# Optimization experiments

Hardware: AMD Instinct MI355X
Metric: run time of the kernel (lower is better)

Reference implementation:

```python
import jax, jax.numpy as jnp
import numpy as np

BETA = 0.9
THR = 1.0
B, T, F, H = 64, 256, 1024, 512

# snntorch heaviside spike with ATan surrogate gradient (alpha=2.0, snntorch default)
@jax.custom_vjp
def spike_fn(u):
    return (u > 0).astype(u.dtype)

def _spike_fwd(u):
    return spike_fn(u), u

def _spike_bwd(u, g):
    alpha = 2.0
    grad = (alpha / 2.0) / (1.0 + (jnp.pi / 2.0 * alpha * u) ** 2)
    return (g * grad,)

spike_fn.defvjp(_spike_fwd, _spike_bwd)


def setup_inputs() -> dict:
    key = jax.random.key(0)
    ks = jax.random.split(key, 12)
    s = 0.05
    return {
        "f_f": jax.random.normal(ks[0], (B, T, F), dtype=jnp.float32),
        "seq_len": jnp.full((B,), T, dtype=jnp.int64),
        "Wf": jax.random.normal(ks[1], (H, F), dtype=jnp.float32) * s,
        "bf": jnp.zeros((H,), jnp.float32),
        "W1": jax.random.normal(ks[2], (H, H), dtype=jnp.float32) * s,
        "b1": jnp.zeros((H,), jnp.float32),
        "W2": jax.random.normal(ks[3], (H, H), dtype=jnp.float32) * s,
        "b2": jnp.zeros((H,), jnp.float32),
        "Mw1": jax.random.normal(ks[4], (512, H), dtype=jnp.float32) * s,
        "Mb1": jnp.zeros((512,), jnp.float32),
        "Mw2": jax.random.normal(ks[5], (32, 512), dtype=jnp.float32) * s,
        "Mb2": jnp.zeros((32,), jnp.float32),
        "Mw3": jax.random.normal(ks[6], (1, 32), dtype=jnp.float32) * s,
        "Mb3": jnp.zeros((1,), jnp.float32),
    }


def _forward(f_f, Wf, bf, W1, b1, W2, b2, Mw1, Mb1, Mw2, Mb2, Mw3, Mb3):
    h = f_f @ Wf.T + bf            # [B,T,H] fc_f
    x1 = h @ W1.T + b1             # layer-1 linear drive precomputed (state-independent)

    def step(carry, x1_t):
        m1, m2 = carry
        # snntorch Leaky (subtract reset): reset from previous mem's spike
        r1 = spike_fn(m1 - THR)
        m1 = BETA * m1 + x1_t - r1 * THR
        s1 = spike_fn(m1 - THR)
        x2 = s1 @ W2.T + b2        # layer-2 linear on spikes (dropout=identity, eval)
        r2 = spike_fn(m2 - THR)
        m2 = BETA * m2 + x2 - r2 * THR
        s2 = spike_fn(m2 - THR)
        return (m1, m2), s2

    init = (jnp.zeros((B, H), h.dtype), jnp.zeros((B, H), h.dtype))
    _, spk = jax.lax.scan(step, init, jnp.swapaxes(x1, 0, 1))  # [T,B,H]
    spk = jnp.swapaxes(spk, 0, 1)                              # [B,T,H]

    z = jax.nn.relu(spk @ Mw1.T + Mb1)
    z = z @ Mw2.T + Mb2
    logits = jax.nn.sigmoid((z @ Mw3.T + Mb3).squeeze(-1))     # [B,T]

    # filter: top-(seq_len//16 + 1) mean per clip; seq_len == T for all clips
    k = T // 16 + 1
    topv, _ = jax.lax.top_k(logits, k)
    return jnp.mean(topv, axis=-1)                             # [B]


def reference(f_f, seq_len, Wf, bf, W1, b1, W2, b2, Mw1, Mb1, Mw2, Mb2, Mw3, Mb3):
    return _forward(f_f, Wf, bf, W1, b1, W2, b2, Mw1, Mb1, Mw2, Mb2, Mw3, Mb3)
```

## Files before the change

### kernel.cpp

```cpp
#include <hip/hip_runtime.h>
#include <math.h>

#define BETA 0.9f
#define THR 1.0f

constexpr int B_ = 64, T_ = 256, F_ = 1024, H_ = 512;
constexpr int M_ = B_ * T_;

typedef float f32x4 __attribute__((ext_vector_type(4)));
typedef short short8 __attribute__((ext_vector_type(8)));
typedef _Float16 half8 __attribute__((ext_vector_type(8)));
typedef unsigned short us4 __attribute__((ext_vector_type(4)));
typedef unsigned short us8 __attribute__((ext_vector_type(8)));
typedef unsigned short ushort_t;

static __device__ __forceinline__ unsigned short f2bf(float x) {
    unsigned b = __builtin_bit_cast(unsigned, x);
    unsigned r = (b + 0x7FFFu + ((b >> 16) & 1u)) >> 16;
    return (unsigned short)r;
}
static __device__ __forceinline__ float bf2f(unsigned short u) {
    unsigned v = ((unsigned)u) << 16;
    return __builtin_bit_cast(float, v);
}
static __device__ __forceinline__ unsigned short f2h(float x) {
    _Float16 h = (_Float16)x;
    return __builtin_bit_cast(unsigned short, h);
}
static __device__ __forceinline__ float h2f(unsigned short u) {
    return (float)__builtin_bit_cast(_Float16, u);
}
static __device__ __forceinline__ int swz(int r) {
    return ((r >> 2) & 3) ^ (r & 3);
}

#define GLDS(srcp, dstp)                                                      \
    __builtin_amdgcn_global_load_lds(                                         \
        (const __attribute__((address_space(1))) unsigned int*)(srcp),        \
        (__attribute__((address_space(3))) unsigned int*)(dstp), 16, 0, 0)

template <int AF32>
__global__ __launch_bounds__(512, 4) void gemm_scan(
    const void* __restrict__ Asrc, const ushort_t* __restrict__ Bp,
    const float* __restrict__ bias, ushort_t* __restrict__ Sout, int K) {
    constexpr int BUF = 20480;
    __shared__ ushort_t lds[2 * BUF];

    const int tid = threadIdx.x;
    const int w = tid >> 6, l = tid & 63;
    const int flat = blockIdx.y * gridDim.x + blockIdx.x;
    const int clip = ((flat >> 6) << 3) | (flat & 7);
    const int strip = (flat >> 3) & 7;
    const int n0 = strip * 64;
    const int m0 = clip * 256;

    f32x4 acc[2][4];
#pragma unroll
    for (int mi = 0; mi < 2; ++mi)
#pragma unroll
        for (int ni = 0; ni < 4; ++ni) acc[mi][ni] = (f32x4){0.f, 0.f, 0.f, 0.f};

    const int c0 = l >> 4;
    const int schunk = (l & 7) ^ ((l >> 3) & 7);

    f32x4 areg[4][2];

    auto stageB = [&](int buf, int k0) {
        const int r = w * 8 + (l >> 3);
        GLDS(Bp + (size_t)(n0 + r) * K + k0 + schunk * 8,
             &lds[buf + 16384 + w * 512]);
    };
    auto stageA16 = [&](int buf, int k0) {
#pragma unroll
        for (int j = 0; j < 4; ++j) {
            const int seg = w * 4 + j;
            const int r = seg * 8 + (l >> 3);
            GLDS((const ushort_t*)Asrc + (size_t)(m0 + r) * K + k0 + schunk * 8,
                 &lds[buf + seg * 512]);
        }
    };
    auto loadA32 = [&](int k0) {
#pragma unroll
        for (int j = 0; j < 4; ++j) {
            const int r = j * 64 + (tid >> 3);
            const float* src =
                (const float*)Asrc + (size_t)(m0 + r) * K + k0 + (tid & 7) * 8;
            areg[j][0] = *(const f32x4*)src;
            areg[j][1] = *(const f32x4*)(src + 4);
        }
    };
    auto writeA32 = [&](int buf) {
#pragma unroll
        for (int j = 0; j < 4; ++j) {
            const int r = j * 64 + (tid >> 3);
            us8 hv;
#pragma unroll
            for (int e = 0; e < 4; ++e) {
                hv[e] = f2h(areg[j][0][e]);
                hv[e + 4] = f2h(areg[j][1][e]);
            }
            const int pos = (tid & 7) ^ (r & 7);
            *(us8*)&lds[buf + r * 64 + pos * 8] = hv;
        }
    };

    const int nt = K / 64;
    if constexpr (AF32) {
        loadA32(0);
        writeA32(0);
    } else {
        stageA16(0, 0);
    }
    stageB(0, 0);

    for (int t = 0; t < nt; ++t) {
        const int cur = (t & 1) * BUF;
        const int nxt = BUF - cur;
        __syncthreads();
        const bool more = (t + 1 < nt);
        if (more) {
            if constexpr (AF32) {
                loadA32((t + 1) * 64);
                stageB(nxt, (t + 1) * 64);
            } else {
                stageA16(nxt, (t + 1) * 64);
                stageB(nxt, (t + 1) * 64);
            }
        }

#pragma unroll
        for (int kh = 0; kh < 2; ++kh) {
            half8 aa[2], bb[4];
            const int q = kh * 4 + c0;
#pragma unroll
            for (int mi = 0; mi < 2; ++mi) {
                const int r = w * 32 + mi * 16 + (l & 15);
                const int off = cur + r * 64 + ((q ^ (l & 7)) * 8);
                aa[mi] = __builtin_bit_cast(half8, *(const short8*)&lds[off]);
            }
#pragma unroll
            for (int ni = 0; ni < 4; ++ni) {
                const int r = ni * 16 + (l & 15);
                const int off = cur + 16384 + r * 64 + ((q ^ (l & 7)) * 8);
                bb[ni] = __builtin_bit_cast(half8, *(const short8*)&lds[off]);
            }
#pragma unroll
            for (int mi = 0; mi < 2; ++mi)
#pragma unroll
                for (int ni = 0; ni < 4; ++ni)
                    acc[mi][ni] = __builtin_amdgcn_mfma_f32_16x16x32_f16(
                        aa[mi], bb[ni], acc[mi][ni], 0, 0, 0);
        }

        if constexpr (AF32) {
            if (more) writeA32(nxt);
        }
    }

    float bv[4];
#pragma unroll
    for (int ni = 0; ni < 4; ++ni) bv[ni] = bias[n0 + ni * 16 + (l & 15)];
#pragma unroll
    for (int mi = 0; mi < 2; ++mi) {
        const int t0 = w * 32 + mi * 16 + ((l >> 4) << 2);
#pragma unroll
        for (int ni = 0; ni < 4; ++ni) {
            const int h = ni * 16 + (l & 15);
#pragma unroll
            for (int r = 0; r < 4; ++r)
                lds[(t0 + r) * 66 + h] = f2h(acc[mi][ni][r] + bv[ni]);
        }
    }
    __syncthreads();

    if (tid < 64) {
        const int h = tid;
        ushort_t* sp = Sout + (size_t)m0 * 512 + n0 + h;
        float m = 0.f;
#pragma unroll 4
        for (int t = 0; t < T_; ++t) {
            const float xv = h2f(lds[t * 66 + h]);
            const float r = (m - THR > 0.f) ? THR : 0.f;
            m = BETA * m + xv - r;
            sp[(size_t)t * 512] = (m - THR > 0.f) ? (ushort_t)0x3C00 : (ushort_t)0;
        }
    }
}

__global__ __launch_bounds__(256) void gemm_mil(
    const ushort_t* __restrict__ Ap, const ushort_t* __restrict__ Bp,
    const float* __restrict__ bias, const float* __restrict__ Uv,
    float* __restrict__ part, int N, int K) {
    constexpr int BUF = 16384;
    __shared__ ushort_t lds[2 * BUF];

    const int tid = threadIdx.x;
    const int w = tid >> 6, l = tid & 63;
    const int flat = blockIdx.y * gridDim.x + blockIdx.x;
    const int mt = ((flat >> 5) << 3) | (flat & 7);
    const int st = (flat >> 3) & 3;
    const int n0 = st * 128;
    const int m0 = mt * 128;
    const int wr = w >> 1, wc = w & 1;

    f32x4 acc[4][4];
#pragma unroll
    for (int mi = 0; mi < 4; ++mi)
#pragma unroll
        for (int ni = 0; ni < 4; ++ni) acc[mi][ni] = (f32x4){0.f, 0.f, 0.f, 0.f};

    const int c0 = l >> 4;
    const int schunk = (l & 7) ^ ((l >> 3) & 7);

    auto stage = [&](int buf, int k0) {
#pragma unroll
        for (int j = 0; j < 8; ++j) {
            const int g = w * 8 + j;
            const int seg = g & 15;
            const int r = seg * 8 + (l >> 3);
            const ushort_t* pl = (g < 16) ? Ap : Bp;
            const int rb = (g < 16) ? m0 : n0;
            GLDS(pl + (size_t)(rb + r) * K + k0 + schunk * 8,
                 &lds[buf + g * 512]);
        }
    };

    const int nt = K / 64;
    stage(0, 0);
    for (int t = 0; t < nt; ++t) {
        const int cur = (t & 1) * BUF;
        const int nxt = BUF - cur;
        __syncthreads();
        if (t + 1 < nt) stage(nxt, (t + 1) * 64);

#pragma unroll
        for (int kh = 0; kh < 2; ++kh) {
            half8 aa[4], bb[4];
            const int q = kh * 4 + c0;
#pragma unroll
            for (int mi = 0; mi < 4; ++mi) {
                const int r = wr * 64 + mi * 16 + (l & 15);
                const int off = cur + r * 64 + ((q ^ (l & 7)) * 8);
                aa[mi] = __builtin_bit_cast(half8, *(const short8*)&lds[off]);
            }
#pragma unroll
            for (int ni = 0; ni < 4; ++ni) {
                const int r = wc * 64 + ni * 16 + (l & 15);
                const int off = cur + 8192 + r * 64 + ((q ^ (l & 7)) * 8);
                bb[ni] = __builtin_bit_cast(half8, *(const short8*)&lds[off]);
            }
#pragma unroll
            for (int mi = 0; mi < 4; ++mi)
#pragma unroll
                for (int ni = 0; ni < 4; ++ni)
                    acc[mi][ni] = __builtin_amdgcn_mfma_f32_16x16x32_f16(
                        aa[mi], bb[ni], acc[mi][ni], 0, 0, 0);
        }
    }

    float bv[4], uc[4];
#pragma unroll
    for (int ni = 0; ni < 4; ++ni) {
        const int col = n0 + wc * 64 + ni * 16 + (l & 15);
        bv[ni] = bias[col];
        uc[ni] = Uv[col];
    }
    const int strip = (n0 >> 6) + wc;
#pragma unroll
    for (int mi = 0; mi < 4; ++mi) {
        float p[4];
#pragma unroll
        for (int r = 0; r < 4; ++r) {
            float s = 0.f;
#pragma unroll
            for (int ni = 0; ni < 4; ++ni)
                s += fmaxf(acc[mi][ni][r] + bv[ni], 0.f) * uc[ni];
            p[r] = s;
        }
#pragma unroll
        for (int off = 1; off <= 8; off <<= 1)
#pragma unroll
            for (int r = 0; r < 4; ++r) p[r] += __shfl_xor(p[r], off);
        if ((l & 15) == 0) {
            const int row0 = m0 + wr * 64 + mi * 16 + ((l >> 4) << 2);
#pragma unroll
            for (int r = 0; r < 4; ++r)
                part[(size_t)strip * M_ + row0 + r] = p[r];
        }
    }
}

__global__ __launch_bounds__(256) void gemm_bf16_wc(
    const ushort_t* __restrict__ Ah, const ushort_t* __restrict__ Al,
    const ushort_t* __restrict__ Bh, const ushort_t* __restrict__ Bl,
    ushort_t* __restrict__ Cout, int N, int K) {
    __shared__ ushort_t lds[4 * 4096];

    const int tid = threadIdx.x;
    const int w = tid >> 6, l = tid & 63;
    const int nwg = gridDim.x * gridDim.y;
    const int flat = blockIdx.y * gridDim.x + blockIdx.x;
    const int wg = (flat & 7) * (nwg >> 3) + (flat >> 3);
    const int n0 = (wg % gridDim.x) * 128;
    const int m0 = (wg / gridDim.x) * 128;
    const int wr = w >> 1, wc = w & 1;

    f32x4 acc[4][4];
#pragma unroll
    for (int mi = 0; mi < 4; ++mi)
#pragma unroll
        for (int ni = 0; ni < 4; ++ni) acc[mi][ni] = (f32x4){0.f, 0.f, 0.f, 0.f};

    const int c0 = l >> 4;
    for (int k0 = 0; k0 < K; k0 += 32) {
        __syncthreads();
#pragma unroll
        for (int j = 0; j < 8; ++j) {
            const int g = w * 8 + j;
            const int p = g >> 3, seg = g & 7;
            const int r = seg * 16 + (l >> 2);
            const int ch = (l & 3) ^ swz(r);
            const ushort_t* pl = (p == 0) ? Ah : (p == 1) ? Al : (p == 2) ? Bh : Bl;
            const int rb = (p < 2) ? m0 : n0;
            GLDS(pl + (size_t)(rb + r) * K + k0 + ch * 8,
                 &lds[p * 4096 + seg * 512]);
        }
        __syncthreads();

        short8 ah[4], al[4], bh[4], bl[4];
#pragma unroll
        for (int mi = 0; mi < 4; ++mi) {
            const int r = wr * 64 + mi * 16 + (l & 15);
            const int off = r * 32 + ((c0 ^ swz(r)) * 8);
            ah[mi] = *(const short8*)&lds[off];
            al[mi] = *(const short8*)&lds[4096 + off];
        }
#pragma unroll
        for (int ni = 0; ni < 4; ++ni) {
            const int r = wc * 64 + ni * 16 + (l & 15);
            const int off = r * 32 + ((c0 ^ swz(r)) * 8);
            bh[ni] = *(const short8*)&lds[8192 + off];
            bl[ni] = *(const short8*)&lds[12288 + off];
        }
#pragma unroll
        for (int mi = 0; mi < 4; ++mi)
#pragma unroll
            for (int ni = 0; ni < 4; ++ni) {
                acc[mi][ni] = __builtin_amdgcn_mfma_f32_16x16x32_bf16(
                    ah[mi], bh[ni], acc[mi][ni], 0, 0, 0);
                acc[mi][ni] = __builtin_amdgcn_mfma_f32_16x16x32_bf16(
                    ah[mi], bl[ni], acc[mi][ni], 0, 0, 0);
                acc[mi][ni] = __builtin_amdgcn_mfma_f32_16x16x32_bf16(
                    al[mi], bh[ni], acc[mi][ni], 0, 0, 0);
            }
    }

#pragma unroll
    for (int ni = 0; ni < 4; ++ni) {
        const int col = n0 + wc * 64 + ni * 16 + (l & 15);
#pragma unroll
        for (int mi = 0; mi < 4; ++mi) {
            const int row0 = m0 + wr * 64 + mi * 16 + ((l >> 4) << 2);
#pragma unroll
            for (int r = 0; r < 4; ++r)
                Cout[(size_t)(row0 + r) * N + col] = f2h(acc[mi][ni][r]);
        }
    }
}

__global__ __launch_bounds__(256) void prep_small(
    const float* __restrict__ W1, const float* __restrict__ W2,
    const float* __restrict__ Mw1, const float* __restrict__ bfv,
    const float* __restrict__ b1, const float* __restrict__ Mw2,
    const float* __restrict__ Mb2, const float* __restrict__ Mw3,
    const float* __restrict__ Mb3, const float* __restrict__ Wf,
    ushort_t* __restrict__ w1h, ushort_t* __restrict__ w1l,
    ushort_t* __restrict__ w2f, ushort_t* __restrict__ m1f,
    float* __restrict__ bc, float* __restrict__ uc,
    ushort_t* __restrict__ wfTh, ushort_t* __restrict__ wfTl) {
    __shared__ float tile[32][33];
    const int blk = blockIdx.x;
    const int tid = threadIdx.x;
    if (blk < 256) {
        const int i = blk * 256 + tid;
        f32x4 v = ((const f32x4*)W1)[i];
        us4 h, ll;
#pragma unroll
        for (int e = 0; e < 4; ++e) {
            const unsigned short hb = f2bf(v[e]);
            h[e] = hb;
            ll[e] = f2bf(v[e] - bf2f(hb));
        }
        ((us4*)w1h)[i] = h;
        ((us4*)w1l)[i] = ll;
    } else if (blk < 512) {
        const int i = (blk - 256) * 256 + tid;
        f32x4 v = ((const f32x4*)W2)[i];
        us4 h;
#pragma unroll
        for (int e = 0; e < 4; ++e) h[e] = f2h(v[e]);
        ((us4*)w2f)[i] = h;
    } else if (blk < 768) {
        const int i = (blk - 512) * 256 + tid;
        f32x4 v = ((const f32x4*)Mw1)[i];
        us4 h;
#pragma unroll
        for (int e = 0; e < 4; ++e) h[e] = f2h(v[e]);
        ((us4*)m1f)[i] = h;
    } else if (blk < 896) {
        const int w = tid >> 6, l = tid & 63;
        const int j = (blk - 768) * 4 + w;
        const float* row = W1 + (size_t)j * 512;
        float a = 0.f;
#pragma unroll
        for (int i = 0; i < 8; ++i) a += row[l + i * 64] * bfv[l + i * 64];
#pragma unroll
        for (int off = 32; off >= 1; off >>= 1) a += __shfl_xor(a, off);
        if (l == 0) bc[j] = a + b1[j];
    } else if (blk < 898) {
        const int j = (blk - 896) * 256 + tid;
        float a = 0.f;
        for (int i = 0; i < 32; ++i) a += Mw3[i] * Mw2[(size_t)i * 512 + j];
        uc[j] = a;
        if (j == 0) {
            float c = Mb3[0];
            for (int i = 0; i < 32; ++i) c += Mw3[i] * Mb2[i];
            uc[512] = c;
        }
    } else {
        const int idx = blk - 898;
        const int k0 = (idx & 31) * 32;
        const int i0 = (idx >> 5) * 32;
        const int tx = tid & 31;
        const int ty = tid >> 5;
#pragma unroll
        for (int e = 0; e < 4; ++e) {
            const int i = ty + e * 8;
            tile[i][tx] = Wf[(size_t)(i0 + i) * 1024 + k0 + tx];
        }
        __syncthreads();
#pragma unroll
        for (int e = 0; e < 4; ++e) {
            const int kk = ty + e * 8;
            const float v = tile[tx][kk];
            const unsigned short h = f2bf(v);
            wfTh[(size_t)(k0 + kk) * 512 + i0 + tx] = h;
            wfTl[(size_t)(k0 + kk) * 512 + i0 + tx] = f2bf(v - bf2f(h));
        }
    }
}

__global__ __launch_bounds__(64) void tail_topk(const float* __restrict__ part,
                                                const float* __restrict__ uc,
                                                float* __restrict__ out) {
    const int b = blockIdx.x;
    const int lane = threadIdx.x;
    const float c = uc[512];
    float v[4];
#pragma unroll
    for (int i = 0; i < 4; ++i) {
        const int row = b * T_ + lane + i * 64;
        float a = 0.f;
#pragma unroll
        for (int s = 0; s < 8; ++s) a += part[(size_t)s * M_ + row];
        v[i] = a + c;
    }
    float sum = 0.f;
    for (int iter = 0; iter < 17; ++iter) {
        float mv = v[0];
        int mslot = 0;
#pragma unroll
        for (int i = 1; i < 4; ++i)
            if (v[i] > mv) { mv = v[i]; mslot = i; }
        float bv = mv;
        int bl = lane, bs = mslot;
#pragma unroll
        for (int off = 32; off >= 1; off >>= 1) {
            const float ov = __shfl_xor(bv, off);
            const int ol = __shfl_xor(bl, off);
            const int os = __shfl_xor(bs, off);
            if (ov > bv || (ov == bv && ol < bl)) { bv = ov; bl = ol; bs = os; }
        }
        sum += 1.f / (1.f + expf(-bv));
        if (lane == bl) v[bs] = -1e30f;
    }
    if (lane == 0) out[b] = sum * (1.f / 17.f);
}

extern "C" void kernel_launch(void* const* d_in, const int* in_sizes, int n_in,
                              void* d_out, int out_size, void* d_ws, size_t ws_size,
                              hipStream_t stream) {
    const float* f_f = (const float*)d_in[0];
    const float* Wf  = (const float*)d_in[2];
    const float* bf  = (const float*)d_in[3];
    const float* W1  = (const float*)d_in[4];
    const float* b1  = (const float*)d_in[5];
    const float* W2  = (const float*)d_in[6];
    const float* b2  = (const float*)d_in[7];
    const float* Mw1 = (const float*)d_in[8];
    const float* Mb1 = (const float*)d_in[9];
    const float* Mw2 = (const float*)d_in[10];
    const float* Mb2 = (const float*)d_in[11];
    const float* Mw3 = (const float*)d_in[12];
    const float* Mb3 = (const float*)d_in[13];
    float* out = (float*)d_out;

    char* ws = (char*)d_ws;
    const size_t NE = (size_t)M_ * H_;
    ushort_t* sbuf1 = (ushort_t*)ws;
    ushort_t* sbuf2 = sbuf1 + NE;
    ushort_t* w1h = sbuf2 + NE;
    ushort_t* w1l = w1h + 262144;
    ushort_t* w2f = w1l + 262144;
    ushort_t* m1f = w2f + 262144;
    ushort_t* wfTh = m1f + 262144;
    ushort_t* wfTl = wfTh + 524288;
    ushort_t* wcf = wfTl + 524288;
    float* bc = (float*)(wcf + 524288);
    float* uc = bc + 512;
    float* part = uc + 513 + 63;

    const dim3 blk(256);

    prep_small<<<dim3(1410), blk, 0, stream>>>(W1, W2, Mw1, bf, b1, Mw2, Mb2,
                                               Mw3, Mb3, Wf, w1h, w1l, w2f,
                                               m1f, bc, uc, wfTh, wfTl);

    gemm_bf16_wc<<<dim3(8, 4), blk, 0, stream>>>(w1h, w1l, wfTh, wfTl, wcf,
                                                 1024, 512);
    gemm_scan<1><<<dim3(8, 64), dim3(512), 0, stream>>>(f_f, wcf, bc, sbuf1,
                                                        1024);
    gemm_scan<0><<<dim3(8, 64), dim3(512), 0, stream>>>(sbuf1, w2f, b2, sbuf2,
                                                        512);
    gemm_mil<<<dim3(4, 128), blk, 0, stream>>>(sbuf2, m1f, Mb1, uc, part,
                                               512, 512);
    tail_topk<<<dim3(B_), dim3(64), 0, stream>>>(part, uc, out);
}
```

Baseline: 112.3 us.

## Double-buffer split-bf16 GEMM with 64-wide K tiles and raise MFMA wave priority

Rewrites the bf16 hi/lo GEMM main loop to double-buffer LDS with K tiles of 64, so global-to-LDS loads for the next tile overlap the MFMAs on the current one, and drops one barrier per iteration. It changes the LDS swizzle, raises launch bounds to one block, and removes the workgroup remapping used for L2 locality. It also wraps the MFMA blocks in all GEMMs with s_setprio to favour math-issuing waves. The cost is more LDS per block (128KB), which limits occupancy, and possibly worse cache locality without the remap.

```diff
diff --git a/kernel.cpp b/kernel.cpp
--- a/kernel.cpp
+++ b/kernel.cpp
@@ -144,12 +144,14 @@
                 const int off = cur + 16384 + r * 64 + ((q ^ (l & 7)) * 8);
                 bb[ni] = __builtin_bit_cast(half8, *(const short8*)&lds[off]);
             }
+            __builtin_amdgcn_s_setprio(1);
 #pragma unroll
             for (int mi = 0; mi < 2; ++mi)
 #pragma unroll
                 for (int ni = 0; ni < 4; ++ni)
                     acc[mi][ni] = __builtin_amdgcn_mfma_f32_16x16x32_f16(
                         aa[mi], bb[ni], acc[mi][ni], 0, 0, 0);
+            __builtin_amdgcn_s_setprio(0);
         }
 
         if constexpr (AF32) {
@@ -249,12 +251,14 @@
                 const int off = cur + 8192 + r * 64 + ((q ^ (l & 7)) * 8);
                 bb[ni] = __builtin_bit_cast(half8, *(const short8*)&lds[off]);
             }
+            __builtin_amdgcn_s_setprio(1);
 #pragma unroll
             for (int mi = 0; mi < 4; ++mi)
 #pragma unroll
                 for (int ni = 0; ni < 4; ++ni)
                     acc[mi][ni] = __builtin_amdgcn_mfma_f32_16x16x32_f16(
                         aa[mi], bb[ni], acc[mi][ni], 0, 0, 0);
+            __builtin_amdgcn_s_setprio(0);
         }
     }
 
@@ -290,19 +294,18 @@
     }
 }
 
-__global__ __launch_bounds__(256) void gemm_bf16_wc(
+__global__ __launch_bounds__(256, 1) void gemm_bf16_wc(
     const ushort_t* __restrict__ Ah, const ushort_t* __restrict__ Al,
     const ushort_t* __restrict__ Bh, const ushort_t* __restrict__ Bl,
     ushort_t* __restrict__ Cout, int N, int K) {
-    __shared__ ushort_t lds[4 * 4096];
+    constexpr int BUF = 32768;
+    __shared__ ushort_t lds[2 * BUF];
 
     const int tid = threadIdx.x;
     const int w = tid >> 6, l = tid & 63;
-    const int nwg = gridDim.x * gridDim.y;
     const int flat = blockIdx.y * gridDim.x + blockIdx.x;
-    const int wg = (flat & 7) * (nwg >> 3) + (flat >> 3);
-    const int n0 = (wg % gridDim.x) * 128;
-    const int m0 = (wg / gridDim.x) * 128;
+    const int n0 = (flat % gridDim.x) * 128;
+    const int m0 = (flat / gridDim.x) * 128;
     const int wr = w >> 1, wc = w & 1;
 
     f32x4 acc[4][4];
@@ -312,47 +315,61 @@
         for (int ni = 0; ni < 4; ++ni) acc[mi][ni] = (f32x4){0.f, 0.f, 0.f, 0.f};
 
     const int c0 = l >> 4;
-    for (int k0 = 0; k0 < K; k0 += 32) {
-        __syncthreads();
-#pragma unroll
-        for (int j = 0; j < 8; ++j) {
-            const int g = w * 8 + j;
-            const int p = g >> 3, seg = g & 7;
-            const int r = seg * 16 + (l >> 2);
-            const int ch = (l & 3) ^ swz(r);
+    const int schunk = (l & 7) ^ ((l >> 3) & 7);
+
+    auto stage = [&](int buf, int k0) {
+#pragma unroll
+        for (int j = 0; j < 16; ++j) {
+            const int g = w * 16 + j;
+            const int p = g >> 4, seg = g & 15;
+            const int r = seg * 8 + (l >> 3);
             const ushort_t* pl = (p == 0) ? Ah : (p == 1) ? Al : (p == 2) ? Bh : Bl;
             const int rb = (p < 2) ? m0 : n0;
-            GLDS(pl + (size_t)(rb + r) * K + k0 + ch * 8,
-                 &lds[p * 4096 + seg * 512]);
-        }
+            GLDS(pl + (size_t)(rb + r) * K + k0 + schunk * 8,
+                 &lds[buf + g * 512]);
+        }
+    };
+
+    const int nt = K / 64;
+    stage(0, 0);
+    for (int t = 0; t < nt; ++t) {
+        const int cur = (t & 1) * BUF;
+        const int nxt = BUF - cur;
         __syncthreads();
-
-        short8 ah[4], al[4], bh[4], bl[4];
-#pragma unroll
-        for (int mi = 0; mi < 4; ++mi) {
-            const int r = wr * 64 + mi * 16 + (l & 15);
-            const int off = r * 32 + ((c0 ^ swz(r)) * 8);
-            ah[mi] = *(const short8*)&lds[off];
-            al[mi] = *(const short8*)&lds[4096 + off];
-        }
-#pragma unroll
-        for (int ni = 0; ni < 4; ++ni) {
-            const int r = wc * 64 + ni * 16 + (l & 15);
-            const int off = r * 32 + ((c0 ^ swz(r)) * 8);
-            bh[ni] = *(const short8*)&lds[8192 + off];
-            bl[ni] = *(const short8*)&lds[12288 + off];
-        }
-#pragma unroll
-        for (int mi = 0; mi < 4; ++mi)
+        if (t + 1 < nt) stage(nxt, (t + 1) * 64);
+
+#pragma unroll
+        for (int kh = 0; kh < 2; ++kh) {
+            short8 ah[4], al[4], bh[4], bl[4];
+            const int q = kh * 4 + c0;
+#pragma unroll
+            for (int mi = 0; mi < 4; ++mi) {
+                const int r = wr * 64 + mi * 16 + (l & 15);
+                const int off = r * 64 + ((q ^ (l & 7)) * 8);
+                ah[mi] = *(const short8*)&lds[cur + off];
+                al[mi] = *(const short8*)&lds[cur + 8192 + off];
+            }
 #pragma unroll
             for (int ni = 0; ni < 4; ++ni) {
-                acc[mi][ni] = __builtin_amdgcn_mfma_f32_16x16x32_bf16(
-                    ah[mi], bh[ni], acc[mi][ni], 0, 0, 0);
-                acc[mi][ni] = __builtin_amdgcn_mfma_f32_16x16x32_bf16(
-                    ah[mi], bl[ni], acc[mi][ni], 0, 0, 0);
-                acc[mi][ni] = __builtin_amdgcn_mfma_f32_16x16x32_bf16(
-                    al[mi], bh[ni], acc[mi][ni], 0, 0, 0);
-            }
+                const int r = wc * 64 + ni * 16 + (l & 15);
+                const int off = r * 64 + ((q ^ (l & 7)) * 8);
+                bh[ni] = *(const short8*)&lds[cur + 16384 + off];
+                bl[ni] = *(const short8*)&lds[cur + 24576 + off];
+            }
+            __builtin_amdgcn_s_setprio(1);
+#pragma unroll
+            for (int mi = 0; mi < 4; ++mi)
+#pragma unroll
+                for (int ni = 0; ni < 4; ++ni) {
+                    acc[mi][ni] = __builtin_amdgcn_mfma_f32_16x16x32_bf16(
+                        ah[mi], bh[ni], acc[mi][ni], 0, 0, 0);
+                    acc[mi][ni] = __builtin_amdgcn_mfma_f32_16x16x32_bf16(
+                        ah[mi], bl[ni], acc[mi][ni], 0, 0, 0);
+                    acc[mi][ni] = __builtin_amdgcn_mfma_f32_16x16x32_bf16(
+                        al[mi], bh[ni], acc[mi][ni], 0, 0, 0);
+                }
+            __builtin_amdgcn_s_setprio(0);
+        }
     }
 
 #pragma unroll
```

New measurement: 111.5 us, median of 2. About the same (-0.7%).
